# Performance work log

Measured on AMD Instinct MI355X. Metric: run time of the kernel, lower is better.

## Reference

```python
import jax, jax.numpy as jnp
import numpy as np

E = 6            # number of residual adapter experts / event groups
MAX_SCALE = 0.05
RESIDUAL_SCALE = 1.0
EPS = 1e-12      # F.normalize eps


def setup_inputs() -> dict:
    key = jax.random.key(0)
    ks = jax.random.split(key, 8)
    B, L, D, H, T = 4, 1024, 768, 1536, 32
    seq_embeddings = jax.random.normal(ks[0], (B, L, D), dtype=jnp.float32)
    next_type_ids = jax.random.randint(ks[1], (B, L), 0, T, dtype=jnp.int32)
    # Adapter bank params (6 two-layer MLPs). Original zero-inits W2/b2; we use
    # small random values so the math is exercised.
    W1 = jax.random.normal(ks[2], (E, D, H), dtype=jnp.float32) * 0.02
    b1 = jax.random.normal(ks[3], (E, H), dtype=jnp.float32) * 0.02
    W2 = jax.random.normal(ks[4], (E, H, D), dtype=jnp.float32) * 0.02
    b2 = jax.random.normal(ks[5], (E, D), dtype=jnp.float32) * 0.02
    raw_alpha = jnp.full((E,), -4.0, dtype=jnp.float32)
    # build_event_type_to_group_tensor stand-in: event type -> one of 6 groups
    event_type_to_group = (jnp.arange(T, dtype=jnp.int32) % E)
    return {"seq_embeddings": seq_embeddings, "next_type_ids": next_type_ids,
            "W1": W1, "b1": b1, "W2": W2, "b2": b2,
            "raw_alpha": raw_alpha, "event_type_to_group": event_type_to_group}


def reference(seq_embeddings, next_type_ids, W1, b1, W2, b2, raw_alpha, event_type_to_group):
    x = seq_embeddings                                  # [B, L, D]
    T = event_type_to_group.shape[0]
    safe = jnp.clip(next_type_ids.astype(jnp.int32), 0, T - 1)
    group_ids = event_type_to_group[safe]               # [B, L] in [0, 6)
    # Dense compute of all 6 adapters (dropout is identity in eval mode)
    h = jax.nn.relu(jnp.einsum('bld,edh->bleh', x, W1) + b1)   # [B, L, 6, H]
    residuals = jnp.einsum('bleh,ehd->bled', h, W2) + b2       # [B, L, 6, D]
    # Gather the chosen expert's residual per token
    idx = group_ids[..., None, None]                           # [B, L, 1, 1]
    residual = jnp.take_along_axis(residuals, idx, axis=2)[:, :, 0, :]  # [B, L, D]
    alpha_all = MAX_SCALE * jax.nn.sigmoid(raw_alpha)          # [6]
    alpha = alpha_all[group_ids][..., None]                    # [B, L, 1]
    out = x + RESIDUAL_SCALE * alpha * residual
    norm = jnp.linalg.norm(out, axis=-1, keepdims=True)
    out = out / jnp.maximum(norm, EPS)
    return out
```

## Files before the change

kernel.cpp:

```cpp
#include <hip/hip_runtime.h>
#include <hip/hip_bf16.h>
#include <stdint.h>

#define NTOK 4096
#define DDIM 768
#define HDIM 1536
#define NEXP 6
#define NTYPE 32
#define PADROWS 4224

typedef __bf16 bf16x8 __attribute__((ext_vector_type(8)));
typedef float f32x4 __attribute__((ext_vector_type(4)));

static __device__ __forceinline__ unsigned short f2bf(float f) {
  union { float f; unsigned u; } v; v.f = f;
  unsigned r = v.u + 0x7FFFu + ((v.u >> 16) & 1u);
  return (unsigned short)(r >> 16);
}

static __device__ __forceinline__ void gload_lds16(const void* g, void* lds) {
  auto* g1 = reinterpret_cast<const __attribute__((address_space(1))) uint32_t*>(
      reinterpret_cast<uintptr_t>(g));
  auto* l3 = reinterpret_cast<__attribute__((address_space(3))) uint32_t*>(
      (uint32_t)reinterpret_cast<uintptr_t>(lds));
  __builtin_amdgcn_global_load_lds(g1, l3, 16, 0, 0);
}

__global__ void bucket_kernel(const int* __restrict__ ids, const int* __restrict__ ev2g,
                              int* __restrict__ perm, int* __restrict__ meta) {
  __shared__ int s_ev2g[NTYPE];
  __shared__ int s_cnt[NEXP];
  __shared__ int s_off[NEXP];
  __shared__ int s_cur[NEXP];
  const int tid = threadIdx.x;
  if (tid < NTYPE) s_ev2g[tid] = ev2g[tid];
  if (tid < NEXP) { s_cnt[tid] = 0; s_cur[tid] = 0; }
  __syncthreads();
  int g[4];
  #pragma unroll
  for (int i = 0; i < 4; ++i) {
    int idx = tid * 4 + i;
    int t = ids[idx];
    t = t < 0 ? 0 : (t > NTYPE - 1 ? NTYPE - 1 : t);
    g[i] = s_ev2g[t];
    atomicAdd(&s_cnt[g[i]], 1);
  }
  __syncthreads();
  if (tid == 0) {
    int off = 0, nt = 0;
    int* table = meta + 21;
    for (int e = 0; e < NEXP; ++e) {
      s_off[e] = off;
      int c = s_cnt[e];
      for (int t = 0; t * 128 < c; ++t) {
        int rem = c - t * 128;
        table[nt * 3 + 0] = e;
        table[nt * 3 + 1] = off + t * 128;
        table[nt * 3 + 2] = rem < 128 ? rem : 128;
        ++nt;
      }
      off += c;
    }
    meta[20] = nt;
  }
  __syncthreads();
  #pragma unroll
  for (int i = 0; i < 4; ++i) {
    int idx = tid * 4 + i;
    int pos = s_off[g[i]] + atomicAdd(&s_cur[g[i]], 1);
    perm[pos] = idx;
  }
}

__global__ void xgather_kernel(const float* __restrict__ x, const int* __restrict__ perm,
                               unsigned short* __restrict__ xg) {
  int row = blockIdx.x;
  int t = threadIdx.x;
  int src = perm[row];
  float4 v = reinterpret_cast<const float4*>(x + (size_t)src * DDIM)[t];
  ushort4 o;
  o.x = f2bf(v.x); o.y = f2bf(v.y); o.z = f2bf(v.z); o.w = f2bf(v.w);
  reinterpret_cast<ushort4*>(xg + (size_t)row * DDIM)[t] = o;
}

__global__ __launch_bounds__(256)
void transpose_kernel(const float* __restrict__ W1, const float* __restrict__ W2,
                      unsigned short* __restrict__ w1t, unsigned short* __restrict__ w2t) {
  __shared__ float tile[64][65];
  const int z = blockIdx.z;
  const float* src;
  unsigned short* dst;
  int R, C, bx, by;
  if (z < 6) {
    src = W1 + (size_t)z * 768 * 1536; dst = w1t + (size_t)z * 768 * 1536;
    R = 768; C = 1536; bx = blockIdx.x; by = blockIdx.y;
  } else {
    src = W2 + (size_t)(z - 6) * 768 * 1536; dst = w2t + (size_t)(z - 6) * 768 * 1536;
    R = 1536; C = 768; bx = blockIdx.y; by = blockIdx.x;
  }
  const int r0 = by * 64, c0 = bx * 64;
  const int t = threadIdx.x;
  const int lr = t >> 4;
  const int lc = (t & 15) << 2;
  #pragma unroll
  for (int i = 0; i < 4; ++i) {
    float4 v = *reinterpret_cast<const float4*>(src + (size_t)(r0 + i * 16 + lr) * C + c0 + lc);
    tile[i * 16 + lr][lc]     = v.x;
    tile[i * 16 + lr][lc + 1] = v.y;
    tile[i * 16 + lr][lc + 2] = v.z;
    tile[i * 16 + lr][lc + 3] = v.w;
  }
  __syncthreads();
  const int l8 = (t & 7) << 3;
  #pragma unroll
  for (int p = 0; p < 2; ++p) {
    int j = p * 32 + (t >> 3);
    union { unsigned short u[8]; uint4 v; } pk;
    #pragma unroll
    for (int k = 0; k < 8; ++k) pk.u[k] = f2bf(tile[l8 + k][j]);
    *reinterpret_cast<uint4*>(dst + (size_t)(c0 + j) * R + r0 + l8) = pk.v;
  }
}

template <int K, int BN, int NT, int WMW, int WNW, bool PASS2>
__global__ __launch_bounds__(512, 4)
void gemm_kernel(const unsigned short* __restrict__ A,
                 const unsigned short* __restrict__ Bw,
                 const float* __restrict__ bias,
                 const int* __restrict__ meta,
                 const int* __restrict__ perm,
                 const float* __restrict__ x,
                 const float* __restrict__ raw_alpha,
                 unsigned short* __restrict__ hout,
                 float* __restrict__ out)
{
  constexpr int BM = 128;
  constexpr int NDIM = NT * BN;
  constexpr int MFR = BM / (16 * WMW);
  constexpr int NFR = BN / (16 * WNW);
  constexpr int NK = K / 64;
  constexpr int ACH = BM / 64;
  constexpr int BCH = BN / 64;
  static_assert(WMW * WNW == 8, "8 waves");

  const int nwg = 40 * NT;
  const int q = nwg >> 3;
  const int vid = (blockIdx.x & 7) * q + (blockIdx.x >> 3);
  const int nt = vid / 40;
  const int mt = vid % 40;
  if (mt >= meta[20]) return;
  const int* table = meta + 21;
  const int e = table[mt * 3 + 0], base = table[mt * 3 + 1], cnt = table[mt * 3 + 2];

  __shared__ __align__(16) unsigned short As[2][BM * 64];
  __shared__ __align__(16) unsigned short Bs[2][BN * 64];

  const int tid = threadIdx.x;
  const int wave = tid >> 6, lane = tid & 63;
  const int wm = wave / WNW, wn = wave % WNW;

  const unsigned short* Abase = A + (size_t)base * K;
  const unsigned short* Bbase = Bw + ((size_t)e * NDIM + (size_t)nt * BN) * K;

  f32x4 acc[MFR][NFR];
  #pragma unroll
  for (int i = 0; i < MFR; ++i)
    #pragma unroll
    for (int j = 0; j < NFR; ++j) acc[i][j] = (f32x4){0.f, 0.f, 0.f, 0.f};

  int aRow[ACH], aElem[ACH], aLds[ACH];
  #pragma unroll
  for (int i = 0; i < ACH; ++i) {
    int chunk = i * 512 + tid;
    int o = chunk * 16;
    int row = o >> 7;
    int inb = (o & 127) ^ ((row & 7) << 4);
    aRow[i] = row; aElem[i] = inb >> 1;
    aLds[i] = (i * 512 + wave * 64) * 16;
  }
  int bRow[BCH], bElem[BCH], bLds[BCH];
  #pragma unroll
  for (int i = 0; i < BCH; ++i) {
    int chunk = i * 512 + tid;
    int o = chunk * 16;
    int row = o >> 7;
    int inb = (o & 127) ^ ((row & 7) << 4);
    bRow[i] = row; bElem[i] = inb >> 1;
    bLds[i] = (i * 512 + wave * 64) * 16;
  }

  #pragma unroll
  for (int i = 0; i < ACH; ++i)
    gload_lds16(Abase + (size_t)aRow[i] * K + aElem[i], (char*)As[0] + aLds[i]);
  #pragma unroll
  for (int i = 0; i < BCH; ++i)
    gload_lds16(Bbase + (size_t)bRow[i] * K + bElem[i], (char*)Bs[0] + bLds[i]);
  __syncthreads();

  int cur = 0;
  for (int kt = 0; kt < NK; ++kt) {
    if (kt + 1 < NK) {
      const int k0 = (kt + 1) * 64;
      #pragma unroll
      for (int i = 0; i < ACH; ++i)
        gload_lds16(Abase + (size_t)aRow[i] * K + k0 + aElem[i], (char*)As[cur ^ 1] + aLds[i]);
      #pragma unroll
      for (int i = 0; i < BCH; ++i)
        gload_lds16(Bbase + (size_t)bRow[i] * K + k0 + bElem[i], (char*)Bs[cur ^ 1] + bLds[i]);
    }
    #pragma unroll
    for (int ks = 0; ks < 2; ++ks) {
      bf16x8 av[MFR], bv[NFR];
      const int kb = ks * 64 + ((lane >> 4) << 4);
      #pragma unroll
      for (int mi = 0; mi < MFR; ++mi) {
        int row = wm * (MFR * 16) + mi * 16 + (lane & 15);
        int byte = (row * 128 + kb) ^ ((row & 7) << 4);
        av[mi] = *reinterpret_cast<const bf16x8*>((const char*)As[cur] + byte);
      }
      #pragma unroll
      for (int nj = 0; nj < NFR; ++nj) {
        int row = wn * (NFR * 16) + nj * 16 + (lane & 15);
        int byte = (row * 128 + kb) ^ ((row & 7) << 4);
        bv[nj] = *reinterpret_cast<const bf16x8*>((const char*)Bs[cur] + byte);
      }
      #pragma unroll
      for (int mi = 0; mi < MFR; ++mi)
        #pragma unroll
        for (int nj = 0; nj < NFR; ++nj)
          acc[mi][nj] = __builtin_amdgcn_mfma_f32_16x16x32_bf16(av[mi], bv[nj], acc[mi][nj], 0, 0, 0);
    }
    __syncthreads();
    cur ^= 1;
  }

  const int col0 = nt * BN + wn * (NFR * 16);
  if constexpr (!PASS2) {
    #pragma unroll
    for (int nj = 0; nj < NFR; ++nj) {
      int n = col0 + nj * 16 + (lane & 15);
      float bv = bias[e * NDIM + n];
      #pragma unroll
      for (int mi = 0; mi < MFR; ++mi) {
        int rbase = wm * (MFR * 16) + mi * 16 + ((lane >> 4) << 2);
        #pragma unroll
        for (int r = 0; r < 4; ++r) {
          int row = rbase + r;
          if (row < cnt) {
            float v = fmaxf(acc[mi][nj][r] + bv, 0.0f);
            hout[(size_t)(base + row) * NDIM + n] = f2bf(v);
          }
        }
      }
    }
  } else {
    float alpha = 0.05f / (1.0f + expf(-raw_alpha[e]));
    #pragma unroll
    for (int nj = 0; nj < NFR; ++nj) {
      int n = col0 + nj * 16 + (lane & 15);
      float bv = bias[e * NDIM + n];
      #pragma unroll
      for (int mi = 0; mi < MFR; ++mi) {
        int rbase = wm * (MFR * 16) + mi * 16 + ((lane >> 4) << 2);
        #pragma unroll
        for (int r = 0; r < 4; ++r) {
          int row = rbase + r;
          if (row < cnt) {
            int tok = perm[base + row];
            size_t oi = (size_t)tok * DDIM + n;
            out[oi] = x[oi] + alpha * (acc[mi][nj][r] + bv);
          }
        }
      }
    }
  }
}

__global__ void norm_kernel(float* __restrict__ out) {
  const int wave = threadIdx.x >> 6, lane = threadIdx.x & 63;
  const int tok = (blockIdx.x << 2) + wave;
  float4* p = reinterpret_cast<float4*>(out) + (size_t)tok * 192;
  float4 a = p[lane], b = p[lane + 64], c = p[lane + 128];
  float ss = a.x * a.x + a.y * a.y + a.z * a.z + a.w * a.w
           + b.x * b.x + b.y * b.y + b.z * b.z + b.w * b.w
           + c.x * c.x + c.y * c.y + c.z * c.z + c.w * c.w;
  #pragma unroll
  for (int off = 32; off; off >>= 1) ss += __shfl_xor(ss, off);
  const float s = 1.0f / fmaxf(sqrtf(ss), 1e-12f);
  a.x *= s; a.y *= s; a.z *= s; a.w *= s;
  b.x *= s; b.y *= s; b.z *= s; b.w *= s;
  c.x *= s; c.y *= s; c.z *= s; c.w *= s;
  p[lane] = a; p[lane + 64] = b; p[lane + 128] = c;
}


extern "C" void kernel_launch(void* const* d_in, const int* in_sizes, int n_in,
                              void* d_out, int out_size, void* d_ws, size_t ws_size,
                              hipStream_t stream) {
  const float* x      = (const float*)d_in[0];
  const int*   ids    = (const int*)d_in[1];
  const float* W1     = (const float*)d_in[2];
  const float* b1     = (const float*)d_in[3];
  const float* W2     = (const float*)d_in[4];
  const float* b2     = (const float*)d_in[5];
  const float* ralpha = (const float*)d_in[6];
  const int*   ev2g   = (const int*)d_in[7];
  float* out = (float*)d_out;
  char* ws = (char*)d_ws;

  unsigned short* w1t = (unsigned short*)(ws);
  unsigned short* w2t = (unsigned short*)(ws + 14155776);
  unsigned short* xg  = (unsigned short*)(ws + 28311552);
  unsigned short* h   = (unsigned short*)(ws + 34799616);
  int* perm = (int*)(ws + 47775744);
  int* meta = (int*)(ws + 47808512);

  bucket_kernel<<<1, 1024, 0, stream>>>(ids, ev2g, perm, meta);
  transpose_kernel<<<dim3(24, 12, 12), 256, 0, stream>>>(W1, W2, w1t, w2t);
  xgather_kernel<<<4096, 192, 0, stream>>>(x, perm, xg);
  gemm_kernel<DDIM, 128, 12, 2, 4, false><<<480, 512, 0, stream>>>(
      xg, w1t, b1, meta, perm, x, ralpha, h, out);
  gemm_kernel<HDIM, 64, 12, 4, 2, true><<<480, 512, 0, stream>>>(
      h, w2t, b2, meta, perm, x, ralpha, nullptr, out);
  norm_kernel<<<1024, 256, 0, stream>>>(out);
}
```

Baseline: 178.3 us.

## Merge bucketing into transpose launch and retile GEMMs to 4-wave 128x128 blocks

Folds the token-bucketing kernel into the weight transpose launch as an extra z-slice, so one launch is removed and the bucketing overlaps the transpose. The xgather kernel now handles four rows per block with one wave per row. Both GEMMs use 256-thread blocks with a 128x128 tile and 4x4 MFMA fragments per wave, giving more register reuse per wave. The second GEMM now runs 240 blocks instead of 480, which risks lower occupancy and less parallelism on that stage.

Measured after the change: 193.8 us. 1.09x slower.

```diff
diff --git a/kernel.cpp b/kernel.cpp
--- a/kernel.cpp
+++ b/kernel.cpp
@@ -26,68 +26,59 @@
   __builtin_amdgcn_global_load_lds(g1, l3, 16, 0, 0);
 }
 
-__global__ void bucket_kernel(const int* __restrict__ ids, const int* __restrict__ ev2g,
-                              int* __restrict__ perm, int* __restrict__ meta) {
-  __shared__ int s_ev2g[NTYPE];
-  __shared__ int s_cnt[NEXP];
-  __shared__ int s_off[NEXP];
-  __shared__ int s_cur[NEXP];
-  const int tid = threadIdx.x;
-  if (tid < NTYPE) s_ev2g[tid] = ev2g[tid];
-  if (tid < NEXP) { s_cnt[tid] = 0; s_cur[tid] = 0; }
-  __syncthreads();
-  int g[4];
-  #pragma unroll
-  for (int i = 0; i < 4; ++i) {
-    int idx = tid * 4 + i;
-    int t = ids[idx];
-    t = t < 0 ? 0 : (t > NTYPE - 1 ? NTYPE - 1 : t);
-    g[i] = s_ev2g[t];
-    atomicAdd(&s_cnt[g[i]], 1);
-  }
-  __syncthreads();
-  if (tid == 0) {
-    int off = 0, nt = 0;
-    int* table = meta + 21;
-    for (int e = 0; e < NEXP; ++e) {
-      s_off[e] = off;
-      int c = s_cnt[e];
-      for (int t = 0; t * 128 < c; ++t) {
-        int rem = c - t * 128;
-        table[nt * 3 + 0] = e;
-        table[nt * 3 + 1] = off + t * 128;
-        table[nt * 3 + 2] = rem < 128 ? rem : 128;
-        ++nt;
-      }
-      off += c;
-    }
-    meta[20] = nt;
-  }
-  __syncthreads();
-  #pragma unroll
-  for (int i = 0; i < 4; ++i) {
-    int idx = tid * 4 + i;
-    int pos = s_off[g[i]] + atomicAdd(&s_cur[g[i]], 1);
-    perm[pos] = idx;
-  }
-}
-
-__global__ void xgather_kernel(const float* __restrict__ x, const int* __restrict__ perm,
-                               unsigned short* __restrict__ xg) {
-  int row = blockIdx.x;
-  int t = threadIdx.x;
-  int src = perm[row];
-  float4 v = reinterpret_cast<const float4*>(x + (size_t)src * DDIM)[t];
-  ushort4 o;
-  o.x = f2bf(v.x); o.y = f2bf(v.y); o.z = f2bf(v.z); o.w = f2bf(v.w);
-  reinterpret_cast<ushort4*>(xg + (size_t)row * DDIM)[t] = o;
-}
-
 __global__ __launch_bounds__(256)
-void transpose_kernel(const float* __restrict__ W1, const float* __restrict__ W2,
-                      unsigned short* __restrict__ w1t, unsigned short* __restrict__ w2t) {
+void prep_kernel(const float* __restrict__ W1, const float* __restrict__ W2,
+                 unsigned short* __restrict__ w1t, unsigned short* __restrict__ w2t,
+                 const int* __restrict__ ids, const int* __restrict__ ev2g,
+                 int* __restrict__ perm, int* __restrict__ meta) {
+  const int z = blockIdx.z;
+  const int t = threadIdx.x;
+  if (z == 12) {
+    if (blockIdx.x != 0 || blockIdx.y != 0) return;
+    __shared__ int s_ev2g[NTYPE];
+    __shared__ int s_cnt[NEXP];
+    __shared__ int s_off[NEXP];
+    __shared__ int s_cur[NEXP];
+    if (t < NTYPE) s_ev2g[t] = ev2g[t];
+    if (t < NEXP) { s_cnt[t] = 0; s_cur[t] = 0; }
+    __syncthreads();
+    int g[16];
+    #pragma unroll
+    for (int i = 0; i < 16; ++i) {
+      int idx = t * 16 + i;
+      int ty = ids[idx];
+      ty = ty < 0 ? 0 : (ty > NTYPE - 1 ? NTYPE - 1 : ty);
+      g[i] = s_ev2g[ty];
+      atomicAdd(&s_cnt[g[i]], 1);
+    }
+    __syncthreads();
+    if (t == 0) {
+      int off = 0, nt = 0;
+      int* table = meta + 21;
+      for (int e = 0; e < NEXP; ++e) {
+        s_off[e] = off;
+        int c = s_cnt[e];
+        for (int k = 0; k * 128 < c; ++k) {
+          int rem = c - k * 128;
+          table[nt * 3 + 0] = e;
+          table[nt * 3 + 1] = off + k * 128;
+          table[nt * 3 + 2] = rem < 128 ? rem : 128;
+          ++nt;
+        }
+        off += c;
+      }
+      meta[20] = nt;
+    }
+    __syncthreads();
+    #pragma unroll
+    for (int i = 0; i < 16; ++i) {
+      int idx = t * 16 + i;
+      int pos = s_off[g[i]] + atomicAdd(&s_cur[g[i]], 1);
+      perm[pos] = idx;
+    }
+    return;
+  }
   __shared__ float tile[64][65];
-  const int z = blockIdx.z;
   const float* src;
   unsigned short* dst;
   int R, C, bx, by;
@@ -99,7 +90,6 @@
     R = 1536; C = 768; bx = blockIdx.y; by = blockIdx.x;
   }
   const int r0 = by * 64, c0 = bx * 64;
-  const int t = threadIdx.x;
   const int lr = t >> 4;
   const int lc = (t & 15) << 2;
   #pragma unroll
@@ -122,8 +112,25 @@
   }
 }
 
-template <int K, int BN, int NT, int WMW, int WNW, bool PASS2>
-__global__ __launch_bounds__(512, 4)
+__global__ __launch_bounds__(256)
+void xgather_kernel(const float* __restrict__ x, const int* __restrict__ perm,
+                    unsigned short* __restrict__ xg) {
+  const int wave = threadIdx.x >> 6, lane = threadIdx.x & 63;
+  const int row = (blockIdx.x << 2) + wave;
+  const int src = perm[row];
+  const float4* in = reinterpret_cast<const float4*>(x + (size_t)src * DDIM);
+  ushort4* outp = reinterpret_cast<ushort4*>(xg + (size_t)row * DDIM);
+  #pragma unroll
+  for (int j = 0; j < 3; ++j) {
+    float4 v = in[lane + j * 64];
+    ushort4 o;
+    o.x = f2bf(v.x); o.y = f2bf(v.y); o.z = f2bf(v.z); o.w = f2bf(v.w);
+    outp[lane + j * 64] = o;
+  }
+}
+
+template <int K, int NT, bool PASS2>
+__global__ __launch_bounds__(256, 2)
 void gemm_kernel(const unsigned short* __restrict__ A,
                  const unsigned short* __restrict__ Bw,
                  const float* __restrict__ bias,
@@ -134,14 +141,9 @@
                  unsigned short* __restrict__ hout,
                  float* __restrict__ out)
 {
-  constexpr int BM = 128;
+  constexpr int BM = 128, BN = 128;
   constexpr int NDIM = NT * BN;
-  constexpr int MFR = BM / (16 * WMW);
-  constexpr int NFR = BN / (16 * WNW);
   constexpr int NK = K / 64;
-  constexpr int ACH = BM / 64;
-  constexpr int BCH = BN / 64;
-  static_assert(WMW * WNW == 8, "8 waves");
 
   const int nwg = 40 * NT;
   const int q = nwg >> 3;
@@ -157,44 +159,34 @@
 
   const int tid = threadIdx.x;
   const int wave = tid >> 6, lane = tid & 63;
-  const int wm = wave / WNW, wn = wave % WNW;
+  const int wm = wave >> 1, wn = wave & 1;
 
   const unsigned short* Abase = A + (size_t)base * K;
   const unsigned short* Bbase = Bw + ((size_t)e * NDIM + (size_t)nt * BN) * K;
 
-  f32x4 acc[MFR][NFR];
-  #pragma unroll
-  for (int i = 0; i < MFR; ++i)
-    #pragma unroll
-    for (int j = 0; j < NFR; ++j) acc[i][j] = (f32x4){0.f, 0.f, 0.f, 0.f};
-
-  int aRow[ACH], aElem[ACH], aLds[ACH];
-  #pragma unroll
-  for (int i = 0; i < ACH; ++i) {
-    int chunk = i * 512 + tid;
+  f32x4 acc[4][4];
+  #pragma unroll
+  for (int i = 0; i < 4; ++i)
+    #pragma unroll
+    for (int j = 0; j < 4; ++j) acc[i][j] = (f32x4){0.f, 0.f, 0.f, 0.f};
+
+  int sRow[4], sElem[4], sLds[4];
+  #pragma unroll
+  for (int i = 0; i < 4; ++i) {
+    int chunk = i * 256 + tid;
     int o = chunk * 16;
     int row = o >> 7;
     int inb = (o & 127) ^ ((row & 7) << 4);
-    aRow[i] = row; aElem[i] = inb >> 1;
-    aLds[i] = (i * 512 + wave * 64) * 16;
-  }
-  int bRow[BCH], bElem[BCH], bLds[BCH];
-  #pragma unroll
-  for (int i = 0; i < BCH; ++i) {
-    int chunk = i * 512 + tid;
-    int o = chunk * 16;
-    int row = o >> 7;
-    int inb = (o & 127) ^ ((row & 7) << 4);
-    bRow[i] = row; bElem[i] = inb >> 1;
-    bLds[i] = (i * 512 + wave * 64) * 16;
-  }
-
-  #pragma unroll
-  for (int i = 0; i < ACH; ++i)
-    gload_lds16(Abase + (size_t)aRow[i] * K + aElem[i], (char*)As[0] + aLds[i]);
-  #pragma unroll
-  for (int i = 0; i < BCH; ++i)
-    gload_lds16(Bbase + (size_t)bRow[i] * K + bElem[i], (char*)Bs[0] + bLds[i]);
+    sRow[i] = row; sElem[i] = inb >> 1;
+    sLds[i] = (i * 256 + wave * 64) * 16;
+  }
+
+  #pragma unroll
+  for (int i = 0; i < 4; ++i)
+    gload_lds16(Abase + (size_t)sRow[i] * K + sElem[i], (char*)As[0] + sLds[i]);
+  #pragma unroll
+  for (int i = 0; i < 4; ++i)
+    gload_lds16(Bbase + (size_t)sRow[i] * K + sElem[i], (char*)Bs[0] + sLds[i]);
   __syncthreads();
 
   int cur = 0;
@@ -202,47 +194,47 @@
     if (kt + 1 < NK) {
       const int k0 = (kt + 1) * 64;
       #pragma unroll
-      for (int i = 0; i < ACH; ++i)
-        gload_lds16(Abase + (size_t)aRow[i] * K + k0 + aElem[i], (char*)As[cur ^ 1] + aLds[i]);
-      #pragma unroll
-      for (int i = 0; i < BCH; ++i)
-        gload_lds16(Bbase + (size_t)bRow[i] * K + k0 + bElem[i], (char*)Bs[cur ^ 1] + bLds[i]);
+      for (int i = 0; i < 4; ++i)
+        gload_lds16(Abase + (size_t)sRow[i] * K + k0 + sElem[i], (char*)As[cur ^ 1] + sLds[i]);
+      #pragma unroll
+      for (int i = 0; i < 4; ++i)
+        gload_lds16(Bbase + (size_t)sRow[i] * K + k0 + sElem[i], (char*)Bs[cur ^ 1] + sLds[i]);
     }
     #pragma unroll
     for (int ks = 0; ks < 2; ++ks) {
-      bf16x8 av[MFR], bv[NFR];
+      bf16x8 av[4], bv[4];
       const int kb = ks * 64 + ((lane >> 4) << 4);
       #pragma unroll
-      for (int mi = 0; mi < MFR; ++mi) {
-        int row = wm * (MFR * 16) + mi * 16 + (lane & 15);
+      for (int mi = 0; mi < 4; ++mi) {
+        int row = wm * 64 + mi * 16 + (lane & 15);
         int byte = (row * 128 + kb) ^ ((row & 7) << 4);
         av[mi] = *reinterpret_cast<const bf16x8*>((const char*)As[cur] + byte);
       }
       #pragma unroll
-      for (int nj = 0; nj < NFR; ++nj) {
-        int row = wn * (NFR * 16) + nj * 16 + (lane & 15);
+      for (int nj = 0; nj < 4; ++nj) {
+        int row = wn * 64 + nj * 16 + (lane & 15);
         int byte = (row * 128 + kb) ^ ((row & 7) << 4);
         bv[nj] = *reinterpret_cast<const bf16x8*>((const char*)Bs[cur] + byte);
       }
       #pragma unroll
-      for (int mi = 0; mi < MFR; ++mi)
+      for (int mi = 0; mi < 4; ++mi)
         #pragma unroll
-        for (int nj = 0; nj < NFR; ++nj)
+        for (int nj = 0; nj < 4; ++nj)
           acc[mi][nj] = __builtin_amdgcn_mfma_f32_16x16x32_bf16(av[mi], bv[nj], acc[mi][nj], 0, 0, 0);
     }
     __syncthreads();
     cur ^= 1;
   }
 
-  const int col0 = nt * BN + wn * (NFR * 16);
+  const int col0 = nt * BN + wn * 64;
   if constexpr (!PASS2) {
     #pragma unroll
-    for (int nj = 0; nj < NFR; ++nj) {
+    for (int nj = 0; nj < 4; ++nj) {
       int n = col0 + nj * 16 + (lane & 15);
       float bv = bias[e * NDIM + n];
       #pragma unroll
-      for (int mi = 0; mi < MFR; ++mi) {
-        int rbase = wm * (MFR * 16) + mi * 16 + ((lane >> 4) << 2);
+      for (int mi = 0; mi < 4; ++mi) {
+        int rbase = wm * 64 + mi * 16 + ((lane >> 4) << 2);
         #pragma unroll
         for (int r = 0; r < 4; ++r) {
           int row = rbase + r;
@@ -256,12 +248,12 @@
   } else {
     float alpha = 0.05f / (1.0f + expf(-raw_alpha[e]));
     #pragma unroll
-    for (int nj = 0; nj < NFR; ++nj) {
+    for (int nj = 0; nj < 4; ++nj) {
       int n = col0 + nj * 16 + (lane & 15);
       float bv = bias[e * NDIM + n];
       #pragma unroll
-      for (int mi = 0; mi < MFR; ++mi) {
-        int rbase = wm * (MFR * 16) + mi * 16 + ((lane >> 4) << 2);
+      for (int mi = 0; mi < 4; ++mi) {
+        int rbase = wm * 64 + mi * 16 + ((lane >> 4) << 2);
         #pragma unroll
         for (int r = 0; r < 4; ++r) {
           int row = rbase + r;
@@ -276,7 +268,8 @@
   }
 }
 
-__global__ void norm_kernel(float* __restrict__ out) {
+__global__ __launch_bounds__(256)
+void norm_kernel(float* __restrict__ out) {
   const int wave = threadIdx.x >> 6, lane = threadIdx.x & 63;
   const int tok = (blockIdx.x << 2) + wave;
   float4* p = reinterpret_cast<float4*>(out) + (size_t)tok * 192;
@@ -315,12 +308,11 @@
   int* perm = (int*)(ws + 47775744);
   int* meta = (int*)(ws + 47808512);
 
-  bucket_kernel<<<1, 1024, 0, stream>>>(ids, ev2g, perm, meta);
-  transpose_kernel<<<dim3(24, 12, 12), 256, 0, stream>>>(W1, W2, w1t, w2t);
-  xgather_kernel<<<4096, 192, 0, stream>>>(x, perm, xg);
-  gemm_kernel<DDIM, 128, 12, 2, 4, false><<<480, 512, 0, stream>>>(
+  prep_kernel<<<dim3(24, 12, 13), 256, 0, stream>>>(W1, W2, w1t, w2t, ids, ev2g, perm, meta);
+  xgather_kernel<<<1024, 256, 0, stream>>>(x, perm, xg);
+  gemm_kernel<DDIM, 12, false><<<480, 256, 0, stream>>>(
       xg, w1t, b1, meta, perm, x, ralpha, h, out);
-  gemm_kernel<HDIM, 64, 12, 4, 2, true><<<480, 512, 0, stream>>>(
+  gemm_kernel<HDIM, 6, true><<<240, 256, 0, stream>>>(
       h, w2t, b2, meta, perm, x, ralpha, nullptr, out);
   norm_kernel<<<1024, 256, 0, stream>>>(out);
 }
```
